# Performance work log

Measured on AMD Instinct MI355X. Metric: run time of the kernel, lower is better.

## Reference

```python
import jax, jax.numpy as jnp
import numpy as np

NUM_LAYERS = 3
IN_C, HID_C, OUT_C = 128, 128, 64
N_NODES, N_EDGES = 100000, 1600000


def setup_inputs() -> dict:
    key = jax.random.key(0)
    ks = jax.random.split(key, 8)
    x = jax.random.normal(ks[0], (N_NODES, IN_C), dtype=jnp.float32)
    edge_index = jax.random.randint(ks[1], (2, N_EDGES), 0, N_NODES, dtype=jnp.int64)
    s_in = 1.0 / np.sqrt(IN_C)
    s_h = 1.0 / np.sqrt(HID_C)
    W_in = jax.random.uniform(ks[2], (IN_C, HID_C), jnp.float32, -s_in, s_in)
    W_convs = jax.random.uniform(ks[3], (NUM_LAYERS, HID_C, HID_C), jnp.float32, -s_h, s_h)
    b_convs = jax.random.uniform(ks[4], (NUM_LAYERS, HID_C), jnp.float32, -s_h, s_h)
    W_fc = jax.random.uniform(ks[5], (HID_C, OUT_C), jnp.float32, -s_h, s_h)
    b_fc = jax.random.uniform(ks[6], (OUT_C,), jnp.float32, -s_h, s_h)
    return {"x": x, "edge_index": edge_index, "W_in": W_in, "W_convs": W_convs,
            "b_convs": b_convs, "W_fc": W_fc, "b_fc": b_fc}


def _g2_tau(x_new, row, col, num_nodes):
    # per-edge squared L2 difference of gated features (p=2)
    d = x_new[row] - x_new[col]            # [E, H]
    diffs = jnp.sum(d * d, axis=-1)        # [E]
    tau_vals = jax.ops.segment_sum(diffs, row, num_segments=num_nodes)
    deg = jax.ops.segment_sum(jnp.ones_like(diffs), row, num_segments=num_nodes) + 1e-10
    return jnp.tanh(tau_vals / deg)[:, None]  # [N, 1]


def reference(x, edge_index, W_in, W_convs, b_convs, W_fc, b_fc):
    row, col = edge_index[0], edge_index[1]
    n = x.shape[0]
    x = x @ W_in                                            # input_fc (no bias)
    for l in range(NUM_LAYERS):
        h = x @ W_convs[l]                                  # GCNConv linear
        agg = jax.ops.segment_sum(h[row], col, num_segments=n) + b_convs[l]
        x_new = jax.nn.relu(agg)
        tau = _g2_tau(x_new, row, col, n)
        x = (1.0 - tau) * x + tau * x_new
    return x @ W_fc + b_fc
```

## Files before the change

### kernel.cpp

```cpp
#include <hip/hip_runtime.h>
#include <hip/hip_bf16.h>

#define N_NODES 100000
#define N_EDGES 1600000
#define HID 128
#define OUTC 64
#define NLAYERS 3

#define M_PAD 100032
#define SCAN_N (2 * N_NODES)
#define SCAN_B 1024
#define SCAN_NB ((SCAN_N + SCAN_B - 1) / SCAN_B)

typedef __attribute__((ext_vector_type(8))) short short8;
typedef __attribute__((ext_vector_type(4))) float f32x4;

__device__ __forceinline__ unsigned short f2b(float f) {
  return __builtin_bit_cast(unsigned short, __float2bfloat16(f));
}
__device__ __forceinline__ float blo(unsigned int u) {
  return __builtin_bit_cast(float, u << 16);
}
__device__ __forceinline__ float bhi(unsigned int u) {
  return __builtin_bit_cast(float, u & 0xffff0000u);
}

__global__ __launch_bounds__(256) void cast_x2_kernel(
    const float* __restrict__ x, unsigned int* __restrict__ xb) {
  const int i2 = blockIdx.x * 256 + threadIdx.x;
  if (i2 >= M_PAD * 64) return;
  unsigned int p = 0;
  if (i2 < N_NODES * 64) {
    const float2 v = reinterpret_cast<const float2*>(x)[i2];
    p = (unsigned)f2b(v.x) | ((unsigned)f2b(v.y) << 16);
  }
  xb[i2] = p;
}

__global__ __launch_bounds__(128) void cast_w_kernel(
    const float* __restrict__ W_in, const float* __restrict__ W_convs,
    const float* __restrict__ W_fc, unsigned short* __restrict__ wt) {
  const int b = blockIdx.x;
  const int k = threadIdx.x;
  const float* src;
  unsigned short* dst;
  int n, N;
  if (b < 128) {
    n = b; N = 128; src = W_in; dst = wt + n * 128;
  } else if (b < 512) {
    const int l = (b - 128) >> 7;
    n = (b - 128) & 127; N = 128;
    src = W_convs + (size_t)l * 16384;
    dst = wt + 16384 * (1 + l) + n * 128;
  } else {
    n = b - 512; N = 64; src = W_fc; dst = wt + 65536 + n * 128;
  }
  dst[k] = f2b(src[k * N + n]);
}

template <int MODE>
__global__ __launch_bounds__(256) void gemm_mfma_kernel(
    const unsigned short* __restrict__ Xb, const unsigned short* __restrict__ Wt,
    const float* __restrict__ bias, float* __restrict__ Y,
    unsigned short* __restrict__ Yb) {
  constexpr int NT = (MODE == 2) ? 4 : 8;
  const int wave = threadIdx.x >> 6;
  const int lane = threadIdx.x & 63;
  const int row0 = blockIdx.x * 64 + wave * 16;
  const int lm = lane & 15;
  const int lk = (lane >> 4) * 8;

  f32x4 acc[NT];
#pragma unroll
  for (int t = 0; t < NT; ++t) acc[t] = {0.f, 0.f, 0.f, 0.f};

  const unsigned short* a_base = Xb + (size_t)(row0 + lm) * 128 + lk;
#pragma unroll
  for (int ki = 0; ki < 4; ++ki) {
    const short8 a = *reinterpret_cast<const short8*>(a_base + ki * 32);
#pragma unroll
    for (int t = 0; t < NT; ++t) {
      const short8 b =
          *reinterpret_cast<const short8*>(Wt + (t * 16 + lm) * 128 + ki * 32 + lk);
      acc[t] = __builtin_amdgcn_mfma_f32_16x16x32_bf16(a, b, acc[t], 0, 0, 0);
    }
  }

  const int orow = row0 + (lane >> 4) * 4;
#pragma unroll
  for (int t = 0; t < NT; ++t) {
#pragma unroll
    for (int r = 0; r < 4; ++r) {
      const int rr = orow + r;
      const int cc = t * 16 + lm;
      const float v = acc[t][r];
      if (MODE == 2) {
        if (rr < N_NODES) Y[(size_t)rr * OUTC + cc] = v + bias[cc];
      } else {
        Yb[(size_t)rr * 128 + cc] = f2b(v);
      }
    }
  }
}

__global__ __launch_bounds__(256) void count_kernel(
    const int* __restrict__ row, const int* __restrict__ col,
    int* __restrict__ counts, unsigned int* __restrict__ ranks) {
  const int e = blockIdx.x * 256 + threadIdx.x;
  if (e >= N_EDGES) return;
  const int pr = atomicAdd(counts + row[e], 1);
  const int pc = atomicAdd(counts + N_NODES + col[e], 1);
  ranks[e] = (unsigned)pr | ((unsigned)pc << 16);
}

__global__ __launch_bounds__(SCAN_B) void scan1_kernel(
    const int* __restrict__ counts, int* __restrict__ incl,
    int* __restrict__ bsum) {
  __shared__ int tmp[SCAN_B];
  const int i = blockIdx.x * SCAN_B + threadIdx.x;
  tmp[threadIdx.x] = (i < SCAN_N) ? counts[i] : 0;
  __syncthreads();
  for (int d = 1; d < SCAN_B; d <<= 1) {
    int t = (threadIdx.x >= d) ? tmp[threadIdx.x - d] : 0;
    __syncthreads();
    tmp[threadIdx.x] += t;
    __syncthreads();
  }
  if (i < SCAN_N) incl[i] = tmp[threadIdx.x];
  if (threadIdx.x == SCAN_B - 1) bsum[blockIdx.x] = tmp[SCAN_B - 1];
}

__global__ __launch_bounds__(256) void scan2_kernel(int* __restrict__ bsum) {
  __shared__ int tmp[256];
  tmp[threadIdx.x] = (threadIdx.x < SCAN_NB) ? bsum[threadIdx.x] : 0;
  __syncthreads();
  for (int d = 1; d < 256; d <<= 1) {
    int t = (threadIdx.x >= d) ? tmp[threadIdx.x - d] : 0;
    __syncthreads();
    tmp[threadIdx.x] += t;
    __syncthreads();
  }
  if (threadIdx.x < SCAN_NB) bsum[threadIdx.x] = tmp[threadIdx.x];
}

__global__ __launch_bounds__(SCAN_B) void scan3_kernel(
    const int* __restrict__ counts, int* __restrict__ incl,
    const int* __restrict__ bsum, int* __restrict__ cur) {
  const int i = blockIdx.x * SCAN_B + threadIdx.x;
  if (i >= SCAN_N) return;
  int v = incl[i] + (blockIdx.x > 0 ? bsum[blockIdx.x - 1] : 0);
  incl[i] = v;
  cur[i] = v - counts[i];
}

__global__ __launch_bounds__(256) void fill_kernel(
    const int* __restrict__ row, const int* __restrict__ col,
    const unsigned int* __restrict__ ranks, const int* __restrict__ cur,
    int* __restrict__ adj) {
  const int e = blockIdx.x * 256 + threadIdx.x;
  if (e >= N_EDGES) return;
  const int r = row[e];
  const int c = col[e];
  const unsigned int u = ranks[e];
  adj[cur[r] + (int)(u & 0xffffu)] = c;
  adj[cur[N_NODES + c] + (int)(u >> 16)] = r;
}

__global__ __launch_bounds__(256) void aggregate_kernel(
    const unsigned int* __restrict__ hb, const int* __restrict__ incl,
    const int* __restrict__ counts, const int* __restrict__ adj,
    const float* __restrict__ b, unsigned int* __restrict__ xnewb) {
  const int g = blockIdx.x * 256 + threadIdx.x;
  const int n = g >> 6;
  if (n >= N_NODES) return;
  const int lane = g & 63;
  const int cnt = counts[N_NODES + n];
  const int start = incl[N_NODES + n] - cnt;
  const int end = start + cnt;

  float a0x = 0.f, a0y = 0.f, a1x = 0.f, a1y = 0.f;
  float a2x = 0.f, a2y = 0.f, a3x = 0.f, a3y = 0.f;
  int i = start;
  for (; i + 3 < end; i += 4) {
    const unsigned int v0 = hb[(size_t)adj[i] * 64 + lane];
    const unsigned int v1 = hb[(size_t)adj[i + 1] * 64 + lane];
    const unsigned int v2 = hb[(size_t)adj[i + 2] * 64 + lane];
    const unsigned int v3 = hb[(size_t)adj[i + 3] * 64 + lane];
    a0x += blo(v0); a0y += bhi(v0);
    a1x += blo(v1); a1y += bhi(v1);
    a2x += blo(v2); a2y += bhi(v2);
    a3x += blo(v3); a3y += bhi(v3);
  }
  for (; i < end; ++i) {
    const unsigned int v0 = hb[(size_t)adj[i] * 64 + lane];
    a0x += blo(v0); a0y += bhi(v0);
  }
  const float2 bb = *reinterpret_cast<const float2*>(b + lane * 2);
  const float ox = fmaxf(((a0x + a1x) + (a2x + a3x)) + bb.x, 0.f);
  const float oy = fmaxf(((a0y + a1y) + (a2y + a3y)) + bb.y, 0.f);
  xnewb[(size_t)n * 64 + lane] = (unsigned)f2b(ox) | ((unsigned)f2b(oy) << 16);
}

__global__ __launch_bounds__(256) void tau_update_kernel(
    const unsigned int* __restrict__ xnewb, const int* __restrict__ incl,
    const int* __restrict__ counts, const int* __restrict__ adj,
    unsigned int* __restrict__ x) {
  const int g = blockIdx.x * 256 + threadIdx.x;
  const int n = g >> 6;
  if (n >= N_NODES) return;
  const int lane = g & 63;
  const int cnt = counts[n];
  const int start = incl[n] - cnt;
  const int end = start + cnt;

  const unsigned int mp = xnewb[(size_t)n * 64 + lane];
  const float mx = blo(mp), my = bhi(mp);

  float s0 = 0.f, s1 = 0.f, s2 = 0.f, s3 = 0.f;
  int i = start;
  for (; i + 3 < end; i += 4) {
    const unsigned int v0 = xnewb[(size_t)adj[i] * 64 + lane];
    const unsigned int v1 = xnewb[(size_t)adj[i + 1] * 64 + lane];
    const unsigned int v2 = xnewb[(size_t)adj[i + 2] * 64 + lane];
    const unsigned int v3 = xnewb[(size_t)adj[i + 3] * 64 + lane];
    const float d0x = mx - blo(v0), d0y = my - bhi(v0);
    const float d1x = mx - blo(v1), d1y = my - bhi(v1);
    const float d2x = mx - blo(v2), d2y = my - bhi(v2);
    const float d3x = mx - blo(v3), d3y = my - bhi(v3);
    s0 += d0x * d0x + d0y * d0y;
    s1 += d1x * d1x + d1y * d1y;
    s2 += d2x * d2x + d2y * d2y;
    s3 += d3x * d3x + d3y * d3y;
  }
  for (; i < end; ++i) {
    const unsigned int v0 = xnewb[(size_t)adj[i] * 64 + lane];
    const float d0x = mx - blo(v0), d0y = my - bhi(v0);
    s0 += d0x * d0x + d0y * d0y;
  }
  float s = (s0 + s1) + (s2 + s3);
  s += __shfl_xor(s, 1);
  s += __shfl_xor(s, 2);
  s += __shfl_xor(s, 4);
  s += __shfl_xor(s, 8);
  s += __shfl_xor(s, 16);
  s += __shfl_xor(s, 32);
  const float tau = tanhf(s / ((float)cnt + 1e-10f));

  const unsigned int xp = x[(size_t)n * 64 + lane];
  const float nx = (1.f - tau) * blo(xp) + tau * mx;
  const float ny = (1.f - tau) * bhi(xp) + tau * my;
  x[(size_t)n * 64 + lane] = (unsigned)f2b(nx) | ((unsigned)f2b(ny) << 16);
}

extern "C" void kernel_launch(void* const* d_in, const int* in_sizes, int n_in,
                              void* d_out, int out_size, void* d_ws,
                              size_t ws_size, hipStream_t stream) {
  const float* x_in = (const float*)d_in[0];
  const int* ei = (const int*)d_in[1];
  const float* W_in = (const float*)d_in[2];
  const float* W_convs = (const float*)d_in[3];
  const float* b_convs = (const float*)d_in[4];
  const float* W_fc = (const float*)d_in[5];
  const float* b_fc = (const float*)d_in[6];
  float* out = (float*)d_out;

  const int* row = ei;
  const int* col = ei + N_EDGES;

  const size_t PF = (size_t)M_PAD * HID;
  unsigned short* xb = (unsigned short*)d_ws;
  unsigned short* xb2 = xb + PF;
  unsigned short* hb = xb2 + PF;
  unsigned short* xnewb = hb + PF;
  unsigned short* wt = xnewb + PF;
  int* counts = (int*)(wt + 73728);
  int* incl = counts + SCAN_N;
  int* cur = incl + SCAN_N;
  int* bsum = cur + SCAN_N;
  unsigned int* ranks = (unsigned int*)(bsum + 1024);
  int* adj = (int*)(ranks + N_EDGES);

  const int GEMM_BLOCKS = M_PAD / 64;
  const int EDGE_BLOCKS = (N_EDGES + 255) / 256;
  const int WAVE_BLOCKS = (N_NODES * 64 + 255) / 256;
  const int CASTX_BLOCKS = (M_PAD * 64) / 256;

  cast_x2_kernel<<<CASTX_BLOCKS, 256, 0, stream>>>(x_in, (unsigned int*)xb);
  cast_w_kernel<<<576, 128, 0, stream>>>(W_in, W_convs, W_fc, wt);

  hipMemsetAsync(counts, 0, SCAN_N * sizeof(int), stream);
  count_kernel<<<EDGE_BLOCKS, 256, 0, stream>>>(row, col, counts, ranks);
  scan1_kernel<<<SCAN_NB, SCAN_B, 0, stream>>>(counts, incl, bsum);
  scan2_kernel<<<1, 256, 0, stream>>>(bsum);
  scan3_kernel<<<SCAN_NB, SCAN_B, 0, stream>>>(counts, incl, bsum, cur);
  fill_kernel<<<EDGE_BLOCKS, 256, 0, stream>>>(row, col, ranks, cur, adj);

  gemm_mfma_kernel<1><<<GEMM_BLOCKS, 256, 0, stream>>>(xb, wt, nullptr, nullptr, xb2);

  for (int l = 0; l < NLAYERS; ++l) {
    const unsigned short* wtl = wt + 16384 * (1 + l);
    const float* bl = b_convs + (size_t)l * HID;

    gemm_mfma_kernel<1><<<GEMM_BLOCKS, 256, 0, stream>>>(xb2, wtl, nullptr, nullptr, hb);
    aggregate_kernel<<<WAVE_BLOCKS, 256, 0, stream>>>(
        (const unsigned int*)hb, incl, counts, adj, bl, (unsigned int*)xnewb);
    tau_update_kernel<<<WAVE_BLOCKS, 256, 0, stream>>>(
        (const unsigned int*)xnewb, incl, counts, adj, (unsigned int*)xb2);
  }

  gemm_mfma_kernel<2><<<GEMM_BLOCKS, 256, 0, stream>>>(xb2, wt + 65536, b_fc, out, nullptr);
}
```

Before: 834.0 us.

## Use FP8 neighbor features for tau, fuse input cast into GEMM, pack CSR segments

The aggregate kernel now also writes an FP8 copy of the gated features, and the tau kernel gathers neighbors from this 1-byte-per-element copy instead of bf16. This halves the bytes of the random neighbor gathers at the cost of lower precision in the squared-difference sum. The separate fp32-to-bf16 input cast kernel is dropped and the first GEMM converts fp32 rows on load. CSR start/count are packed into one int2 array, and the fill kernel handles two edges per thread.

Result: no change. 838.4 us (+0.5%).

```diff
diff --git a/kernel.cpp b/kernel.cpp
--- a/kernel.cpp
+++ b/kernel.cpp
@@ -14,6 +14,7 @@
 
 typedef __attribute__((ext_vector_type(8))) short short8;
 typedef __attribute__((ext_vector_type(4))) float f32x4;
+typedef __attribute__((ext_vector_type(2))) float f32x2;
 
 __device__ __forceinline__ unsigned short f2b(float f) {
   return __builtin_bit_cast(unsigned short, __float2bfloat16(f));
@@ -23,18 +24,6 @@
 }
 __device__ __forceinline__ float bhi(unsigned int u) {
   return __builtin_bit_cast(float, u & 0xffff0000u);
-}
-
-__global__ __launch_bounds__(256) void cast_x2_kernel(
-    const float* __restrict__ x, unsigned int* __restrict__ xb) {
-  const int i2 = blockIdx.x * 256 + threadIdx.x;
-  if (i2 >= M_PAD * 64) return;
-  unsigned int p = 0;
-  if (i2 < N_NODES * 64) {
-    const float2 v = reinterpret_cast<const float2*>(x)[i2];
-    p = (unsigned)f2b(v.x) | ((unsigned)f2b(v.y) << 16);
-  }
-  xb[i2] = p;
 }
 
 __global__ __launch_bounds__(128) void cast_w_kernel(
@@ -60,9 +49,9 @@
 
 template <int MODE>
 __global__ __launch_bounds__(256) void gemm_mfma_kernel(
-    const unsigned short* __restrict__ Xb, const unsigned short* __restrict__ Wt,
-    const float* __restrict__ bias, float* __restrict__ Y,
-    unsigned short* __restrict__ Yb) {
+    const float* __restrict__ Xf, const unsigned short* __restrict__ Xb,
+    const unsigned short* __restrict__ Wt, const float* __restrict__ bias,
+    float* __restrict__ Y, unsigned short* __restrict__ Yb) {
   constexpr int NT = (MODE == 2) ? 4 : 8;
   const int wave = threadIdx.x >> 6;
   const int lane = threadIdx.x & 63;
@@ -74,10 +63,22 @@
 #pragma unroll
   for (int t = 0; t < NT; ++t) acc[t] = {0.f, 0.f, 0.f, 0.f};
 
-  const unsigned short* a_base = Xb + (size_t)(row0 + lm) * 128 + lk;
+  const int arow = row0 + lm;
 #pragma unroll
   for (int ki = 0; ki < 4; ++ki) {
-    const short8 a = *reinterpret_cast<const short8*>(a_base + ki * 32);
+    short8 a;
+    if (MODE == 0) {
+      float av[8];
+      const bool ok = arow < N_NODES;
+#pragma unroll
+      for (int j = 0; j < 8; ++j)
+        av[j] = ok ? Xf[(size_t)arow * 128 + ki * 32 + lk + j] : 0.f;
+#pragma unroll
+      for (int j = 0; j < 8; ++j)
+        a[j] = (short)f2b(av[j]);
+    } else {
+      a = *reinterpret_cast<const short8*>(Xb + (size_t)arow * 128 + ki * 32 + lk);
+    }
 #pragma unroll
     for (int t = 0; t < NT; ++t) {
       const short8 b =
@@ -144,39 +145,41 @@
 }
 
 __global__ __launch_bounds__(SCAN_B) void scan3_kernel(
-    const int* __restrict__ counts, int* __restrict__ incl,
-    const int* __restrict__ bsum, int* __restrict__ cur) {
+    const int* __restrict__ counts, const int* __restrict__ incl,
+    const int* __restrict__ bsum, int2* __restrict__ seg) {
   const int i = blockIdx.x * SCAN_B + threadIdx.x;
   if (i >= SCAN_N) return;
-  int v = incl[i] + (blockIdx.x > 0 ? bsum[blockIdx.x - 1] : 0);
-  incl[i] = v;
-  cur[i] = v - counts[i];
+  const int c = counts[i];
+  const int v = incl[i] + (blockIdx.x > 0 ? bsum[blockIdx.x - 1] : 0);
+  seg[i] = make_int2(v - c, c);
 }
 
 __global__ __launch_bounds__(256) void fill_kernel(
     const int* __restrict__ row, const int* __restrict__ col,
-    const unsigned int* __restrict__ ranks, const int* __restrict__ cur,
+    const unsigned int* __restrict__ ranks, const int2* __restrict__ seg,
     int* __restrict__ adj) {
-  const int e = blockIdx.x * 256 + threadIdx.x;
-  if (e >= N_EDGES) return;
-  const int r = row[e];
-  const int c = col[e];
-  const unsigned int u = ranks[e];
-  adj[cur[r] + (int)(u & 0xffffu)] = c;
-  adj[cur[N_NODES + c] + (int)(u >> 16)] = r;
+  const int p = blockIdx.x * 256 + threadIdx.x;
+  if (p * 2 >= N_EDGES) return;
+  const int2 r2 = reinterpret_cast<const int2*>(row)[p];
+  const int2 c2 = reinterpret_cast<const int2*>(col)[p];
+  const uint2 u2 = reinterpret_cast<const uint2*>(ranks)[p];
+  adj[seg[r2.x].x + (int)(u2.x & 0xffffu)] = c2.x;
+  adj[seg[N_NODES + c2.x].x + (int)(u2.x >> 16)] = r2.x;
+  adj[seg[r2.y].x + (int)(u2.y & 0xffffu)] = c2.y;
+  adj[seg[N_NODES + c2.y].x + (int)(u2.y >> 16)] = r2.y;
 }
 
 __global__ __launch_bounds__(256) void aggregate_kernel(
-    const unsigned int* __restrict__ hb, const int* __restrict__ incl,
-    const int* __restrict__ counts, const int* __restrict__ adj,
-    const float* __restrict__ b, unsigned int* __restrict__ xnewb) {
+    const unsigned int* __restrict__ hb, const int2* __restrict__ seg,
+    const int* __restrict__ adj, const float* __restrict__ b,
+    unsigned int* __restrict__ xnewb, unsigned short* __restrict__ xnew8) {
   const int g = blockIdx.x * 256 + threadIdx.x;
   const int n = g >> 6;
   if (n >= N_NODES) return;
   const int lane = g & 63;
-  const int cnt = counts[N_NODES + n];
-  const int start = incl[N_NODES + n] - cnt;
-  const int end = start + cnt;
+  const int2 sg = seg[N_NODES + n];
+  const int start = sg.x;
+  const int end = sg.x + sg.y;
 
   float a0x = 0.f, a0y = 0.f, a1x = 0.f, a1y = 0.f;
   float a2x = 0.f, a2y = 0.f, a3x = 0.f, a3y = 0.f;
@@ -199,18 +202,21 @@
   const float ox = fmaxf(((a0x + a1x) + (a2x + a3x)) + bb.x, 0.f);
   const float oy = fmaxf(((a0y + a1y) + (a2y + a3y)) + bb.y, 0.f);
   xnewb[(size_t)n * 64 + lane] = (unsigned)f2b(ox) | ((unsigned)f2b(oy) << 16);
+  const unsigned int p8 = __builtin_amdgcn_cvt_pk_fp8_f32(ox, oy, 0u, false);
+  xnew8[(size_t)n * 64 + lane] = (unsigned short)(p8 & 0xffffu);
 }
 
 __global__ __launch_bounds__(256) void tau_update_kernel(
-    const unsigned int* __restrict__ xnewb, const int* __restrict__ incl,
-    const int* __restrict__ counts, const int* __restrict__ adj,
+    const unsigned int* __restrict__ xnewb, const unsigned short* __restrict__ xnew8,
+    const int2* __restrict__ seg, const int* __restrict__ adj,
     unsigned int* __restrict__ x) {
   const int g = blockIdx.x * 256 + threadIdx.x;
   const int n = g >> 6;
   if (n >= N_NODES) return;
   const int lane = g & 63;
-  const int cnt = counts[n];
-  const int start = incl[n] - cnt;
+  const int2 sg = seg[n];
+  const int start = sg.x;
+  const int cnt = sg.y;
   const int end = start + cnt;
 
   const unsigned int mp = xnewb[(size_t)n * 64 + lane];
@@ -219,22 +225,27 @@
   float s0 = 0.f, s1 = 0.f, s2 = 0.f, s3 = 0.f;
   int i = start;
   for (; i + 3 < end; i += 4) {
-    const unsigned int v0 = xnewb[(size_t)adj[i] * 64 + lane];
-    const unsigned int v1 = xnewb[(size_t)adj[i + 1] * 64 + lane];
-    const unsigned int v2 = xnewb[(size_t)adj[i + 2] * 64 + lane];
-    const unsigned int v3 = xnewb[(size_t)adj[i + 3] * 64 + lane];
-    const float d0x = mx - blo(v0), d0y = my - bhi(v0);
-    const float d1x = mx - blo(v1), d1y = my - bhi(v1);
-    const float d2x = mx - blo(v2), d2y = my - bhi(v2);
-    const float d3x = mx - blo(v3), d3y = my - bhi(v3);
+    const unsigned int u0 = xnew8[(size_t)adj[i] * 64 + lane];
+    const unsigned int u1 = xnew8[(size_t)adj[i + 1] * 64 + lane];
+    const unsigned int u2 = xnew8[(size_t)adj[i + 2] * 64 + lane];
+    const unsigned int u3 = xnew8[(size_t)adj[i + 3] * 64 + lane];
+    const f32x2 v0 = __builtin_amdgcn_cvt_pk_f32_fp8(u0, false);
+    const f32x2 v1 = __builtin_amdgcn_cvt_pk_f32_fp8(u1, false);
+    const f32x2 v2 = __builtin_amdgcn_cvt_pk_f32_fp8(u2, false);
+    const f32x2 v3 = __builtin_amdgcn_cvt_pk_f32_fp8(u3, false);
+    const float d0x = mx - v0[0], d0y = my - v0[1];
+    const float d1x = mx - v1[0], d1y = my - v1[1];
+    const float d2x = mx - v2[0], d2y = my - v2[1];
+    const float d3x = mx - v3[0], d3y = my - v3[1];
     s0 += d0x * d0x + d0y * d0y;
     s1 += d1x * d1x + d1y * d1y;
     s2 += d2x * d2x + d2y * d2y;
     s3 += d3x * d3x + d3y * d3y;
   }
   for (; i < end; ++i) {
-    const unsigned int v0 = xnewb[(size_t)adj[i] * 64 + lane];
-    const float d0x = mx - blo(v0), d0y = my - bhi(v0);
+    const unsigned int u0 = xnew8[(size_t)adj[i] * 64 + lane];
+    const f32x2 v0 = __builtin_amdgcn_cvt_pk_f32_fp8(u0, false);
+    const float d0x = mx - v0[0], d0y = my - v0[1];
     s0 += d0x * d0x + d0y * d0y;
   }
   float s = (s0 + s1) + (s2 + s3);
@@ -268,45 +279,47 @@
   const int* col = ei + N_EDGES;
 
   const size_t PF = (size_t)M_PAD * HID;
-  unsigned short* xb = (unsigned short*)d_ws;
-  unsigned short* xb2 = xb + PF;
+  unsigned short* xb2 = (unsigned short*)d_ws;
   unsigned short* hb = xb2 + PF;
   unsigned short* xnewb = hb + PF;
-  unsigned short* wt = xnewb + PF;
+  unsigned short* xnew8 = xnewb + PF;
+  unsigned short* wt = xnew8 + (size_t)N_NODES * 64;
   int* counts = (int*)(wt + 73728);
   int* incl = counts + SCAN_N;
-  int* cur = incl + SCAN_N;
-  int* bsum = cur + SCAN_N;
-  unsigned int* ranks = (unsigned int*)(bsum + 1024);
+  int* bsum = incl + SCAN_N;
+  int2* seg = (int2*)(bsum + 1024);
+  unsigned int* ranks = (unsigned int*)(seg + SCAN_N);
   int* adj = (int*)(ranks + N_EDGES);
 
   const int GEMM_BLOCKS = M_PAD / 64;
   const int EDGE_BLOCKS = (N_EDGES + 255) / 256;
+  const int PAIR_BLOCKS = (N_EDGES / 2 + 255) / 256;
   const int WAVE_BLOCKS = (N_NODES * 64 + 255) / 256;
-  const int CASTX_BLOCKS = (M_PAD * 64) / 256;
-
-  cast_x2_kernel<<<CASTX_BLOCKS, 256, 0, stream>>>(x_in, (unsigned int*)xb);
+
   cast_w_kernel<<<576, 128, 0, stream>>>(W_in, W_convs, W_fc, wt);
 
   hipMemsetAsync(counts, 0, SCAN_N * sizeof(int), stream);
   count_kernel<<<EDGE_BLOCKS, 256, 0, stream>>>(row, col, counts, ranks);
   scan1_kernel<<<SCAN_NB, SCAN_B, 0, stream>>>(counts, incl, bsum);
   scan2_kernel<<<1, 256, 0, stream>>>(bsum);
-  scan3_kernel<<<SCAN_NB, SCAN_B, 0, stream>>>(counts, incl, bsum, cur);
-  fill_kernel<<<EDGE_BLOCKS, 256, 0, stream>>>(row, col, ranks, cur, adj);
-
-  gemm_mfma_kernel<1><<<GEMM_BLOCKS, 256, 0, stream>>>(xb, wt, nullptr, nullptr, xb2);
+  scan3_kernel<<<SCAN_NB, SCAN_B, 0, stream>>>(counts, incl, bsum, seg);
+  fill_kernel<<<PAIR_BLOCKS, 256, 0, stream>>>(row, col, ranks, seg, adj);
+
+  gemm_mfma_kernel<0><<<GEMM_BLOCKS, 256, 0, stream>>>(
+      x_in, nullptr, wt, nullptr, nullptr, xb2);
 
   for (int l = 0; l < NLAYERS; ++l) {
     const unsigned short* wtl = wt + 16384 * (1 + l);
     const float* bl = b_convs + (size_t)l * HID;
 
-    gemm_mfma_kernel<1><<<GEMM_BLOCKS, 256, 0, stream>>>(xb2, wtl, nullptr, nullptr, hb);
+    gemm_mfma_kernel<1><<<GEMM_BLOCKS, 256, 0, stream>>>(
+        nullptr, xb2, wtl, nullptr, nullptr, hb);
     aggregate_kernel<<<WAVE_BLOCKS, 256, 0, stream>>>(
-        (const unsigned int*)hb, incl, counts, adj, bl, (unsigned int*)xnewb);
+        (const unsigned int*)hb, seg, adj, bl, (unsigned int*)xnewb, xnew8);
     tau_update_kernel<<<WAVE_BLOCKS, 256, 0, stream>>>(
-        (const unsigned int*)xnewb, incl, counts, adj, (unsigned int*)xb2);
-  }
-
-  gemm_mfma_kernel<2><<<GEMM_BLOCKS, 256, 0, stream>>>(xb2, wt + 65536, b_fc, out, nullptr);
-}
+        (const unsigned int*)xnewb, xnew8, seg, adj, (unsigned int*)xb2);
+  }
+
+  gemm_mfma_kernel<2><<<GEMM_BLOCKS, 256, 0, stream>>>(
+      nullptr, xb2, wt + 65536, b_fc, out, nullptr);
+}
```
